# Performance work log

Hardware: AMD Instinct MI355X
Metric: run time of the kernel (lower is better)

## Reference

```python
import jax, jax.numpy as jnp
import numpy as np

K = 5       # strip kernel size
DIL = 1     # dilation
G = 4       # groups


def _strip_att(x, conv_w, inside_all, lamb_l, lamb_h, horizontal):
    # x: (n, c, h, w); conv_w: (G*K, c); inside_all: (c,1,1); lamb_*: (c,)
    n, c, h, w = x.shape
    # global avg pool -> 1x1 conv -> tanh filter, shaped (n, G, 1, K, 1, 1)
    f = jnp.tanh(jnp.einsum('nc,oc->no', x.mean(axis=(2, 3)), conv_w))
    f = f.reshape(n, G, 1, K, 1, 1)
    pad = DIL * (K - 1) // 2
    if horizontal:
        xp = jnp.pad(x, ((0, 0), (0, 0), (0, 0), (pad, pad)), mode='reflect')
        # K shifted strips along W (equivalent to F.unfold with kernel (1,K))
        wins = jnp.stack([xp[:, :, :, i * DIL:i * DIL + w] for i in range(K)], axis=2)
        gapx = x.mean(axis=3, keepdims=True)   # (n,c,h,1)
    else:
        xp = jnp.pad(x, ((0, 0), (0, 0), (pad, pad), (0, 0)), mode='reflect')
        wins = jnp.stack([xp[:, :, i * DIL:i * DIL + h, :] for i in range(K)], axis=2)
        gapx = x.mean(axis=2, keepdims=True)   # (n,c,1,w)
    # (n,c,K,h,w) -> (n,G,c//G,K,h,w); weighted sum over kernel positions
    wins = wins.reshape(n, G, c // G, K, h, w)
    out = (wins * f).sum(axis=3).reshape(n, c, h, w)
    out_low = (out * (inside_all + 1.0) - inside_all * gapx) * lamb_l[:, None, None]
    out_high = x * (lamb_h[:, None, None] + 1.0)
    return out_low + out_high


def setup_inputs() -> dict:
    key = jax.random.key(0)
    ks = jax.random.split(key, 11)
    C = 128
    x = jax.random.normal(ks[0], (4, C, 256, 256), dtype=jnp.float32)
    s = 0.1
    return {
        'x': x,
        'conv_h': jax.random.normal(ks[1], (G * K, C), dtype=jnp.float32) * s,
        'inside_h': jax.random.normal(ks[2], (C, 1, 1), dtype=jnp.float32) * s,
        'lamb_l_h': jax.random.normal(ks[3], (C,), dtype=jnp.float32) * s,
        'lamb_h_h': jax.random.normal(ks[4], (C,), dtype=jnp.float32) * s,
        'conv_v': jax.random.normal(ks[5], (G * K, C), dtype=jnp.float32) * s,
        'inside_v': jax.random.normal(ks[6], (C, 1, 1), dtype=jnp.float32) * s,
        'lamb_l_v': jax.random.normal(ks[7], (C,), dtype=jnp.float32) * s,
        'lamb_h_v': jax.random.normal(ks[8], (C,), dtype=jnp.float32) * s,
        'gamma': jax.random.normal(ks[9], (C, 1, 1), dtype=jnp.float32) * s,
        'beta': 1.0 + jax.random.normal(ks[10], (C, 1, 1), dtype=jnp.float32) * s,
    }


def reference(x, conv_h, inside_h, lamb_l_h, lamb_h_h,
              conv_v, inside_v, lamb_l_v, lamb_h_v, gamma, beta):
    out = _strip_att(x, conv_h, inside_h, lamb_l_h, lamb_h_h, horizontal=True)
    out = _strip_att(out, conv_v, inside_v, lamb_l_v, lamb_h_v, horizontal=False)
    return gamma * out + x * beta
```

## Files before the change

### kernel.cpp

```cpp
#include <hip/hip_runtime.h>
#include <math.h>

#define NB   4
#define CC   128
#define HH   256
#define WW   256
#define HWSZ (HH * WW)
#define NC   (NB * CC)
#define GK   20

__device__ __forceinline__ float wave_reduce_sum(float v) {
#pragma unroll
    for (int o = 1; o < 64; o <<= 1) v += __shfl_xor(v, o, 64);
    return v;
}

__global__ __launch_bounds__(256) void k_reduce(const float4* __restrict__ x4,
                                                float* __restrict__ colsum,
                                                float* __restrict__ planesum) {
    const int b = blockIdx.x;
    const int t = threadIdx.x;
    const int wv = t >> 6;
    const int l = t & 63;
    const float4* plane = x4 + (size_t)b * (HWSZ / 4);

    float4 cs = make_float4(0.f, 0.f, 0.f, 0.f);
    for (int hb = 0; hb < HH; hb += 8) {
        float4 v1 = plane[(hb + wv) * (WW / 4) + l];
        float4 v2 = plane[(hb + 4 + wv) * (WW / 4) + l];
        cs.x += v1.x + v2.x;
        cs.y += v1.y + v2.y;
        cs.z += v1.z + v2.z;
        cs.w += v1.w + v2.w;
    }

    __shared__ float colpart[4][WW];
    colpart[wv][4 * l + 0] = cs.x;
    colpart[wv][4 * l + 1] = cs.y;
    colpart[wv][4 * l + 2] = cs.z;
    colpart[wv][4 * l + 3] = cs.w;
    __syncthreads();
    float c = (colpart[0][t] + colpart[1][t]) + (colpart[2][t] + colpart[3][t]);
    colsum[b * WW + t] = c;

    float p = wave_reduce_sum(c);
    __shared__ float pr[4];
    if (l == 0) pr[wv] = p;
    __syncthreads();
    if (t == 0) planesum[b] = (pr[0] + pr[1]) + (pr[2] + pr[3]);
}

__global__ __launch_bounds__(256) void k_small(const float* __restrict__ colsum,
                                               const float* __restrict__ planesum,
                                               const float* __restrict__ conv_h,
                                               const float* __restrict__ inside_h,
                                               const float* __restrict__ lamb_l_h,
                                               const float* __restrict__ lamb_h_h,
                                               const float* __restrict__ conv_v,
                                               float* __restrict__ f_h_out,
                                               float* __restrict__ f_v_out) {
    __shared__ float meanx[NC];
    __shared__ float fh[NB * GK];
    __shared__ float mo1[NC];
    const int t = threadIdx.x;

    for (int i = t; i < NC; i += 256) meanx[i] = planesum[i] * (1.f / HWSZ);
    __syncthreads();

    if (t < NB * GK) {
        const int n = t / GK, o = t % GK;
        float acc = 0.f;
        for (int c = 0; c < CC; ++c) acc += meanx[n * CC + c] * conv_h[o * CC + c];
        float v = tanhf(acc);
        fh[t] = v;
        f_h_out[t] = v;
    }
    __syncthreads();

    for (int i = t; i < NC; i += 256) {
        const int n = i >> 7, c = i & (CC - 1), g = c >> 5;
        const float* f = &fh[n * GK + g * 5];
        const float S = planesum[i];
        const float* col = colsum + i * WW;
        const float c0 = col[0], c1 = col[1], c2 = col[2];
        const float c253 = col[253], c254 = col[254], c255 = col[255];
        const float s0 = S + c1 + c2 - c254 - c255;
        const float s1 = S + c1 - c255;
        const float s2 = S;
        const float s3 = S + c254 - c0;
        const float s4 = S + c253 + c254 - c0 - c1;
        const float convmean =
            (f[0] * s0 + f[1] * s1 + f[2] * s2 + f[3] * s3 + f[4] * s4) * (1.f / HWSZ);
        const float A = (inside_h[c] + 1.f) * lamb_l_h[c];
        const float B = inside_h[c] * lamb_l_h[c];
        const float Cq = lamb_h_h[c] + 1.f;
        mo1[i] = A * convmean + (Cq - B) * meanx[i];
    }
    __syncthreads();

    if (t < NB * GK) {
        const int n = t / GK, o = t % GK;
        float acc = 0.f;
        for (int c = 0; c < CC; ++c) acc += mo1[n * CC + c] * conv_v[o * CC + c];
        f_v_out[t] = tanhf(acc);
    }
}

#define TH 64

__global__ __launch_bounds__(256) void k_main(const float* __restrict__ x,
                                              const float* __restrict__ colsum,
                                              const float* __restrict__ planesum,
                                              const float* __restrict__ f_h,
                                              const float* __restrict__ f_v,
                                              const float* __restrict__ inside_h,
                                              const float* __restrict__ lamb_l_h,
                                              const float* __restrict__ lamb_h_h,
                                              const float* __restrict__ inside_v,
                                              const float* __restrict__ lamb_l_v,
                                              const float* __restrict__ lamb_h_v,
                                              const float* __restrict__ gamma,
                                              const float* __restrict__ beta,
                                              float* __restrict__ out) {
    const int b = blockIdx.x >> 2;
    const int tile = blockIdx.x & 3;
    const int h0 = tile * TH;
    const int n = b >> 7, c = b & (CC - 1), g = c >> 5;
    const int t = threadIdx.x;
    const int wv = t >> 6;
    const int l = t & 63;

    float fh[5], fv[5];
#pragma unroll
    for (int k = 0; k < 5; ++k) {
        fh[k] = f_h[n * GK + g * 5 + k];
        fv[k] = f_v[n * GK + g * 5 + k];
    }
    const float Ah = (inside_h[c] + 1.f) * lamb_l_h[c];
    const float Bh = inside_h[c] * lamb_l_h[c];
    const float Ch = lamb_h_h[c] + 1.f;
    const float Av = (inside_v[c] + 1.f) * lamb_l_v[c];
    const float Bv = inside_v[c] * lamb_l_v[c];
    const float Cv = lamb_h_v[c] + 1.f;
    const float gm = gamma[c], bt = beta[c];
    const float meanx = planesum[b] * (1.f / HWSZ);

    __shared__ float lcol[WW + 4];
    lcol[t + 2] = colsum[b * WW + t] * (1.f / HH);
    if (t < 2) lcol[t] = colsum[b * WW + (2 - t)] * (1.f / HH);
    if (t >= WW - 2) lcol[t + 4] = colsum[b * WW + (2 * WW - 4 - t)] * (1.f / HH);
    __syncthreads();
    float gx[4];
    {
        float q[8];
#pragma unroll
        for (int d = 0; d < 8; ++d) q[d] = lcol[4 * l + d];
#pragma unroll
        for (int d = 0; d < 4; ++d) {
            gx[d] = Ah * (fh[0] * q[d] + fh[1] * q[d + 1] + fh[2] * q[d + 2] +
                          fh[3] * q[d + 3] + fh[4] * q[d + 4]) -
                    Bh * meanx + Ch * q[d + 2];
        }
    }

    __shared__ float hring[16][WW];
    const float* plane = x + (size_t)b * HWSZ;
    float* oplane = out + (size_t)b * HWSZ;

    auto rowptr = [&](int j) -> const float4* {
        int hs = h0 - 4 + 4 * j + wv;
        int hr = hs < 0 ? -hs : (hs > HH - 1 ? 2 * HH - 2 - hs : hs);
        return (const float4*)&plane[hr * WW + 4 * l];
    };

    float4 vnext = *rowptr(0);
    float4 xprev = make_float4(0.f, 0.f, 0.f, 0.f);

    for (int j = 0; j <= 17; ++j) {
        float4 v;
        if (j <= 16) {
            v = vnext;
            if (j < 16) vnext = *rowptr(j + 1);

            float rsum = (v.x + v.y) + (v.z + v.w);
            rsum = wave_reduce_sum(rsum);
            const float gh = rsum * (1.f / WW);

            float xm2 = __shfl_up(v.z, 1);
            float xm1 = __shfl_up(v.w, 1);
            float xp4 = __shfl_down(v.x, 1);
            float xp5 = __shfl_down(v.y, 1);
            if (l == 0)  { xm2 = v.z; xm1 = v.y; }
            if (l == 63) { xp4 = v.z; xp5 = v.y; }

            const float h0v = fh[0] * xm2 + fh[1] * xm1 + fh[2] * v.x + fh[3] * v.y + fh[4] * v.z;
            const float h1v = fh[0] * xm1 + fh[1] * v.x + fh[2] * v.y + fh[3] * v.z + fh[4] * v.w;
            const float h2v = fh[0] * v.x + fh[1] * v.y + fh[2] * v.z + fh[3] * v.w + fh[4] * xp4;
            const float h3v = fh[0] * v.y + fh[1] * v.z + fh[2] * v.w + fh[3] * xp4 + fh[4] * xp5;

            float4 r1;
            r1.x = Ah * h0v - Bh * gh + Ch * v.x;
            r1.y = Ah * h1v - Bh * gh + Ch * v.y;
            r1.z = Ah * h2v - Bh * gh + Ch * v.z;
            r1.w = Ah * h3v - Bh * gh + Ch * v.w;

            const int hs = h0 - 4 + 4 * j + wv;
            *(float4*)&hring[hs & 15][4 * l] = r1;
        }
        __syncthreads();

        if (j >= 2) {
            const int O = h0 - 8 + 4 * j + wv;
            float ax = 0.f, ay = 0.f, az = 0.f, aw = 0.f;
            float4 rc;
#pragma unroll
            for (int k = 0; k < 5; ++k) {
                int vrow = O + k - 2;
                int vr = vrow < 0 ? -vrow : (vrow > HH - 1 ? 2 * HH - 2 - vrow : vrow);
                float4 hv = *(const float4*)&hring[vr & 15][4 * l];
                ax += fv[k] * hv.x;
                ay += fv[k] * hv.y;
                az += fv[k] * hv.z;
                aw += fv[k] * hv.w;
                if (k == 2) rc = hv;
            }
            float4 res;
            res.x = gm * (Av * ax - Bv * gx[0] + Cv * rc.x) + bt * xprev.x;
            res.y = gm * (Av * ay - Bv * gx[1] + Cv * rc.y) + bt * xprev.y;
            res.z = gm * (Av * az - Bv * gx[2] + Cv * rc.z) + bt * xprev.z;
            res.w = gm * (Av * aw - Bv * gx[3] + Cv * rc.w) + bt * xprev.w;
            *(float4*)&oplane[O * WW + 4 * l] = res;
        }

        if (j <= 16) xprev = v;
    }
}

extern "C" void kernel_launch(void* const* d_in, const int* in_sizes, int n_in,
                              void* d_out, int out_size, void* d_ws, size_t ws_size,
                              hipStream_t stream) {
    const float* x        = (const float*)d_in[0];
    const float* conv_h   = (const float*)d_in[1];
    const float* inside_h = (const float*)d_in[2];
    const float* lamb_l_h = (const float*)d_in[3];
    const float* lamb_h_h = (const float*)d_in[4];
    const float* conv_v   = (const float*)d_in[5];
    const float* inside_v = (const float*)d_in[6];
    const float* lamb_l_v = (const float*)d_in[7];
    const float* lamb_h_v = (const float*)d_in[8];
    const float* gamma    = (const float*)d_in[9];
    const float* beta     = (const float*)d_in[10];
    float* out = (float*)d_out;

    float* ws = (float*)d_ws;
    float* colsum   = ws;
    float* planesum = ws + 131072;
    float* f_h      = ws + 131584;
    float* f_v      = ws + 131664;

    k_reduce<<<NC, 256, 0, stream>>>((const float4*)x, colsum, planesum);
    k_small<<<1, 256, 0, stream>>>(colsum, planesum, conv_h, inside_h, lamb_l_h,
                                   lamb_h_h, conv_v, f_h, f_v);
    k_main<<<NC * 4, 256, 0, stream>>>(x, colsum, planesum, f_h, f_v,
                                       inside_h, lamb_l_h, lamb_h_h,
                                       inside_v, lamb_l_v, lamb_h_v,
                                       gamma, beta, out);
}
```

Baseline: 78.71 us.

## Split reduction into row chunks and precompute row sums for main kernel

After: 85.51 us. 1.09x slower.

```diff
diff --git a/kernel.cpp b/kernel.cpp
--- a/kernel.cpp
+++ b/kernel.cpp
@@ -16,22 +16,25 @@
 }
 
 __global__ __launch_bounds__(256) void k_reduce(const float4* __restrict__ x4,
-                                                float* __restrict__ colsum,
-                                                float* __restrict__ planesum) {
-    const int b = blockIdx.x;
+                                                float* __restrict__ rowsum,
+                                                float* __restrict__ colsum_part,
+                                                float* __restrict__ planesum_part) {
+    const int bx = blockIdx.x;
+    const int b = bx >> 2;
+    const int chunk = bx & 3;
     const int t = threadIdx.x;
     const int wv = t >> 6;
     const int l = t & 63;
     const float4* plane = x4 + (size_t)b * (HWSZ / 4);
+    const int r0 = chunk * 64 + wv * 16;
 
     float4 cs = make_float4(0.f, 0.f, 0.f, 0.f);
-    for (int hb = 0; hb < HH; hb += 8) {
-        float4 v1 = plane[(hb + wv) * (WW / 4) + l];
-        float4 v2 = plane[(hb + 4 + wv) * (WW / 4) + l];
-        cs.x += v1.x + v2.x;
-        cs.y += v1.y + v2.y;
-        cs.z += v1.z + v2.z;
-        cs.w += v1.w + v2.w;
+#pragma unroll 4
+    for (int i = 0; i < 16; ++i) {
+        float4 v = plane[(r0 + i) * (WW / 4) + l];
+        cs.x += v.x; cs.y += v.y; cs.z += v.z; cs.w += v.w;
+        float rs = wave_reduce_sum((v.x + v.y) + (v.z + v.w));
+        if (l == 0) rowsum[b * HH + r0 + i] = rs;
     }
 
     __shared__ float colpart[4][WW];
@@ -41,30 +44,38 @@
     colpart[wv][4 * l + 3] = cs.w;
     __syncthreads();
     float c = (colpart[0][t] + colpart[1][t]) + (colpart[2][t] + colpart[3][t]);
-    colsum[b * WW + t] = c;
+    colsum_part[(size_t)b * 4 * WW + chunk * WW + t] = c;
 
     float p = wave_reduce_sum(c);
     __shared__ float pr[4];
     if (l == 0) pr[wv] = p;
     __syncthreads();
-    if (t == 0) planesum[b] = (pr[0] + pr[1]) + (pr[2] + pr[3]);
-}
-
-__global__ __launch_bounds__(256) void k_small(const float* __restrict__ colsum,
-                                               const float* __restrict__ planesum,
+    if (t == 0) planesum_part[b * 4 + chunk] = (pr[0] + pr[1]) + (pr[2] + pr[3]);
+}
+
+__global__ __launch_bounds__(256) void k_small(const float* __restrict__ colsum_part,
+                                               const float* __restrict__ planesum_part,
                                                const float* __restrict__ conv_h,
                                                const float* __restrict__ inside_h,
                                                const float* __restrict__ lamb_l_h,
                                                const float* __restrict__ lamb_h_h,
                                                const float* __restrict__ conv_v,
+                                               float* __restrict__ planesum,
                                                float* __restrict__ f_h_out,
                                                float* __restrict__ f_v_out) {
     __shared__ float meanx[NC];
+    __shared__ float psum[NC];
     __shared__ float fh[NB * GK];
     __shared__ float mo1[NC];
     const int t = threadIdx.x;
 
-    for (int i = t; i < NC; i += 256) meanx[i] = planesum[i] * (1.f / HWSZ);
+    for (int i = t; i < NC; i += 256) {
+        float S = (planesum_part[i * 4 + 0] + planesum_part[i * 4 + 1]) +
+                  (planesum_part[i * 4 + 2] + planesum_part[i * 4 + 3]);
+        psum[i] = S;
+        planesum[i] = S;
+        meanx[i] = S * (1.f / HWSZ);
+    }
     __syncthreads();
 
     if (t < NB * GK) {
@@ -80,10 +91,14 @@
     for (int i = t; i < NC; i += 256) {
         const int n = i >> 7, c = i & (CC - 1), g = c >> 5;
         const float* f = &fh[n * GK + g * 5];
-        const float S = planesum[i];
-        const float* col = colsum + i * WW;
-        const float c0 = col[0], c1 = col[1], c2 = col[2];
-        const float c253 = col[253], c254 = col[254], c255 = col[255];
+        const float S = psum[i];
+        const float* col = colsum_part + (size_t)i * 4 * WW;
+        auto csum = [&](int w) {
+            return (col[0 * WW + w] + col[1 * WW + w]) +
+                   (col[2 * WW + w] + col[3 * WW + w]);
+        };
+        const float c0 = csum(0), c1 = csum(1), c2 = csum(2);
+        const float c253 = csum(253), c254 = csum(254), c255 = csum(255);
         const float s0 = S + c1 + c2 - c254 - c255;
         const float s1 = S + c1 - c255;
         const float s2 = S;
@@ -109,7 +124,8 @@
 #define TH 64
 
 __global__ __launch_bounds__(256) void k_main(const float* __restrict__ x,
-                                              const float* __restrict__ colsum,
+                                              const float* __restrict__ rowsum,
+                                              const float* __restrict__ colsum_part,
                                               const float* __restrict__ planesum,
                                               const float* __restrict__ f_h,
                                               const float* __restrict__ f_v,
@@ -146,9 +162,22 @@
     const float meanx = planesum[b] * (1.f / HWSZ);
 
     __shared__ float lcol[WW + 4];
-    lcol[t + 2] = colsum[b * WW + t] * (1.f / HH);
-    if (t < 2) lcol[t] = colsum[b * WW + (2 - t)] * (1.f / HH);
-    if (t >= WW - 2) lcol[t + 4] = colsum[b * WW + (2 * WW - 4 - t)] * (1.f / HH);
+    {
+        const float* col = colsum_part + (size_t)b * 4 * WW;
+        float cm = ((col[0 * WW + t] + col[1 * WW + t]) +
+                    (col[2 * WW + t] + col[3 * WW + t])) * (1.f / HH);
+        lcol[t + 2] = cm;
+        if (t < 2) {
+            int w = 2 - t;
+            lcol[t] = ((col[0 * WW + w] + col[1 * WW + w]) +
+                       (col[2 * WW + w] + col[3 * WW + w])) * (1.f / HH);
+        }
+        if (t >= WW - 2) {
+            int w = 2 * WW - 4 - t;
+            lcol[t + 4] = ((col[0 * WW + w] + col[1 * WW + w]) +
+                           (col[2 * WW + w] + col[3 * WW + w])) * (1.f / HH);
+        }
+    }
     __syncthreads();
     float gx[4];
     {
@@ -167,24 +196,26 @@
     const float* plane = x + (size_t)b * HWSZ;
     float* oplane = out + (size_t)b * HWSZ;
 
-    auto rowptr = [&](int j) -> const float4* {
+    auto hrOf = [&](int j) -> int {
         int hs = h0 - 4 + 4 * j + wv;
-        int hr = hs < 0 ? -hs : (hs > HH - 1 ? 2 * HH - 2 - hs : hs);
-        return (const float4*)&plane[hr * WW + 4 * l];
+        return hs < 0 ? -hs : (hs > HH - 1 ? 2 * HH - 2 - hs : hs);
     };
 
-    float4 vnext = *rowptr(0);
+    int hrn = hrOf(0);
+    float4 vnext = *(const float4*)&plane[hrn * WW + 4 * l];
+    float ghnext = rowsum[b * HH + hrn];
     float4 xprev = make_float4(0.f, 0.f, 0.f, 0.f);
 
     for (int j = 0; j <= 17; ++j) {
         float4 v;
         if (j <= 16) {
             v = vnext;
-            if (j < 16) vnext = *rowptr(j + 1);
-
-            float rsum = (v.x + v.y) + (v.z + v.w);
-            rsum = wave_reduce_sum(rsum);
-            const float gh = rsum * (1.f / WW);
+            const float gh = ghnext * (1.f / WW);
+            if (j < 16) {
+                hrn = hrOf(j + 1);
+                vnext = *(const float4*)&plane[hrn * WW + 4 * l];
+                ghnext = rowsum[b * HH + hrn];
+            }
 
             float xm2 = __shfl_up(v.z, 1);
             float xm1 = __shfl_up(v.w, 1);
@@ -253,15 +284,18 @@
     float* out = (float*)d_out;
 
     float* ws = (float*)d_ws;
-    float* colsum   = ws;
-    float* planesum = ws + 131072;
-    float* f_h      = ws + 131584;
-    float* f_v      = ws + 131664;
-
-    k_reduce<<<NC, 256, 0, stream>>>((const float4*)x, colsum, planesum);
-    k_small<<<1, 256, 0, stream>>>(colsum, planesum, conv_h, inside_h, lamb_l_h,
-                                   lamb_h_h, conv_v, f_h, f_v);
-    k_main<<<NC * 4, 256, 0, stream>>>(x, colsum, planesum, f_h, f_v,
+    float* rowsum        = ws;
+    float* colsum_part   = ws + 131072;
+    float* planesum_part = ws + 655360;
+    float* planesum      = ws + 657408;
+    float* f_h           = ws + 657920;
+    float* f_v           = ws + 658000;
+
+    k_reduce<<<NC * 4, 256, 0, stream>>>((const float4*)x, rowsum, colsum_part,
+                                         planesum_part);
+    k_small<<<1, 256, 0, stream>>>(colsum_part, planesum_part, conv_h, inside_h,
+                                   lamb_l_h, lamb_h_h, conv_v, planesum, f_h, f_v);
+    k_main<<<NC * 4, 256, 0, stream>>>(x, rowsum, colsum_part, planesum, f_h, f_v,
                                        inside_h, lamb_l_h, lamb_h_h,
                                        inside_v, lamb_l_v, lamb_h_v,
                                        gamma, beta, out);
```
